# Kernel tuning notes

Measured on AMD Instinct MI355X. Metric: run time of the kernel, lower is better.

The kernel has to match this reference:

```python
import jax, jax.numpy as jnp
import numpy as np

# Hardcoded module dims (BClassifier: L=500, D=128, K=1; rehearsal_label=[0,1] => 2 classes)
L = 500
D = 128
NUM_CLASSES = 2
BUFFER_SIZE = 512
PER_CLS = BUFFER_SIZE // NUM_CLASSES  # 256
FEAT = 1024
B = 32
N = 4096
TEMP = 0.5
EPS = 1e-8  # torch cosine_similarity eps


def setup_inputs() -> dict:
    key = jax.random.key(0)
    ks = jax.random.split(key, 12)
    s = 0.02
    return {
        "x": jax.random.normal(ks[0], (B, N, FEAT), jnp.float32),
        "y": jax.random.randint(ks[1], (B,), 0, NUM_CLASSES),
        "W1": jax.random.normal(ks[2], (FEAT, L), jnp.float32) * s,
        "b1": jnp.zeros((L,), jnp.float32),
        "Wa": jax.random.normal(ks[3], (L, D), jnp.float32) * s,
        "ba": jnp.zeros((D,), jnp.float32),
        "Va": jax.random.normal(ks[4], (D, 1), jnp.float32) * s,
        "bv": jnp.zeros((1,), jnp.float32),
        "Wc": jax.random.normal(ks[5], (L, NUM_CLASSES), jnp.float32) * s,
        "bc": jnp.zeros((NUM_CLASSES,), jnp.float32),
        "rehearsal": jax.random.uniform(ks[6], (NUM_CLASSES, PER_CLS, L), jnp.float32),
    }


def _l2norm(v, axis=-1, keepdims=True):
    return jnp.maximum(jnp.linalg.norm(v, axis=axis, keepdims=keepdims), EPS)


def reference(x, y, W1, b1, Wa, ba, Va, bv, Wc, bc, rehearsal):
    # --- attention MIL pooling ---
    H = jax.nn.relu(jnp.einsum("bnf,fl->bnl", x, W1) + b1)          # [B,N,L]
    a = jax.nn.relu(jnp.einsum("bnl,ld->bnd", H, Wa) + ba) @ Va + bv  # [B,N,1]
    A = jax.nn.softmax(a[..., 0], axis=-1)                            # [B,N]
    bag_feat = jnp.einsum("bn,bnl->bl", A, H)                         # [B,L]
    logits_mlp = bag_feat @ Wc + bc                                   # [B,C]

    # --- buffer_update: contrastive loss + reg term ---
    cls_means = jnp.mean(rehearsal, axis=1)                           # [C,L]
    sim = bag_feat @ cls_means.T                                      # [B,C]
    pos = jnp.take_along_axis(sim, y[:, None], axis=1)                # [B,1]
    neg = jnp.take_along_axis(sim, (1 - y)[:, None], axis=1)          # [B,1] (C==2)
    logits = jnp.concatenate([pos, neg], axis=1)
    loss = -jnp.mean(jax.nn.log_softmax(logits / TEMP, axis=1)[:, 0])

    cm_n = cls_means / _l2norm(cls_means)                             # [C,L]
    cc = 1.0 + cm_n @ cm_n.T                                          # [C,C]
    reg = (jnp.sum(cc) - jnp.trace(cc)) / 2.0

    # --- sequential rehearsal scatter update ---
    reh_n = rehearsal / _l2norm(rehearsal)                            # [C,P,L]
    cls_dists = jnp.einsum("cl,cpl->cp", cm_n, reh_n)                 # [C,P]
    bag_n = bag_feat / _l2norm(bag_feat)                              # [B,L]

    def step(carry, inp):
        reh, dists = carry
        xi, xin, ci = inp
        d = jnp.dot(cm_n[ci], xin)                 # cos(cls_means[ci], x_i)
        row = dists[ci]
        idx = jnp.argmin(row)
        mv = row[idx]
        cond = d > mv
        reh = reh.at[ci, idx].set(jnp.where(cond, xi, reh[ci, idx]))
        dists = dists.at[ci, idx].set(jnp.where(cond, d, mv))
        return (reh, dists), None

    (new_rehearsal, _), _ = jax.lax.scan(step, (rehearsal, cls_dists), (bag_feat, bag_n, y))

    return logits_mlp, loss, reg, new_rehearsal
```

## Files before the change

kernel.cpp:

```cpp
#include <hip/hip_runtime.h>


#define EPSF 1e-8f

typedef float v4f __attribute__((ext_vector_type(4)));
typedef short v8s __attribute__((ext_vector_type(8)));

__device__ __forceinline__ unsigned short f2bf(float f) {
  unsigned u = __float_as_uint(f);
  u = (u + 0x7fffu + ((u >> 16) & 1u)) >> 16;
  return (unsigned short)u;
}
__device__ __forceinline__ float bf2f(unsigned short b) {
  return __uint_as_float(((unsigned)b) << 16);
}
__device__ __forceinline__ void gll16(const void* g, void* l) {
  __builtin_amdgcn_global_load_lds((const __attribute__((address_space(1))) void*)g,
                                   (__attribute__((address_space(3))) void*)l, 16, 0, 0);
}

__global__ void k0_w1t(const float* __restrict__ W1, unsigned short* __restrict__ W1T) {
  int idx = blockIdx.x * 256 + threadIdx.x;
  int n = idx >> 10, k = idx & 1023;
  float v = (n < 500) ? W1[k * 500 + n] : 0.f;
  W1T[idx] = f2bf(v);
}
__global__ void k0_wat(const float* __restrict__ Wa, unsigned short* __restrict__ WaT) {
  int idx = blockIdx.x * 256 + threadIdx.x;
  int d = idx >> 9, l = idx & 511;
  float v = (l < 500) ? Wa[l * 128 + d] : 0.f;
  WaT[idx] = f2bf(v);
}

__global__ __launch_bounds__(256) void k1_gemm1(const float* __restrict__ x,
    const unsigned short* __restrict__ W1T, const float* __restrict__ b1,
    unsigned short* __restrict__ H) {
  __shared__ float As[128 * 64];
  __shared__ unsigned short Bs[128 * 64];
  int bid = blockIdx.x;
  int n0 = (bid & 3) * 128;
  size_t m0 = (size_t)(bid >> 2) * 128;
  int tid = threadIdx.x;
  int lane = tid & 63, wv = tid >> 6;
  int wm = (wv >> 1) * 64, wn = (wv & 1) * 64;
  int l15 = lane & 15, quad = lane >> 4;
  v4f acc[4][4];
  for (int i = 0; i < 4; i++)
    for (int j = 0; j < 4; j++) acc[i][j] = (v4f)(0.f);

  for (int kt = 0; kt < 1024; kt += 64) {
    const float* gA = x + m0 * 1024 + kt;
    const unsigned short* gB = W1T + (size_t)n0 * 1024 + kt;
#pragma unroll
    for (int p = 0; p < 8; p++) {
      int ci = p * 256 + tid;
      gll16(gA + (size_t)(ci >> 4) * 1024 + (ci & 15) * 4, As + ci * 4);
    }
#pragma unroll
    for (int p = 0; p < 4; p++) {
      int ci = p * 256 + tid;
      gll16(gB + (size_t)(ci >> 3) * 1024 + (ci & 7) * 8, Bs + ci * 8);
    }
    __syncthreads();
#pragma unroll
    for (int kk = 0; kk < 64; kk += 32) {
      v8s af[4], bf[4];
#pragma unroll
      for (int mi = 0; mi < 4; mi++) {
        const float* p = As + (wm + mi * 16 + l15) * 64 + kk + quad * 8;
        v4f lo = *(const v4f*)p;
        v4f hi = *(const v4f*)(p + 4);
        v8s t;
        t[0] = (short)f2bf(lo.x); t[1] = (short)f2bf(lo.y);
        t[2] = (short)f2bf(lo.z); t[3] = (short)f2bf(lo.w);
        t[4] = (short)f2bf(hi.x); t[5] = (short)f2bf(hi.y);
        t[6] = (short)f2bf(hi.z); t[7] = (short)f2bf(hi.w);
        af[mi] = t;
      }
#pragma unroll
      for (int ni = 0; ni < 4; ni++)
        bf[ni] = *(const v8s*)(Bs + (wn + ni * 16 + l15) * 64 + kk + quad * 8);
#pragma unroll
      for (int mi = 0; mi < 4; mi++)
#pragma unroll
        for (int ni = 0; ni < 4; ni++)
          acc[mi][ni] = __builtin_amdgcn_mfma_f32_16x16x32_bf16(af[mi], bf[ni], acc[mi][ni], 0, 0, 0);
    }
    __syncthreads();
  }
#pragma unroll
  for (int mi = 0; mi < 4; mi++) {
#pragma unroll
    for (int ni = 0; ni < 4; ni++) {
      int col = n0 + wn + ni * 16 + l15;
      float bias = (col < 500) ? b1[col] : 0.f;
#pragma unroll
      for (int r = 0; r < 4; r++) {
        size_t row = m0 + wm + mi * 16 + quad * 4 + r;
        float v = (col < 500) ? fmaxf(acc[mi][ni][r] + bias, 0.f) : 0.f;
        H[row * 512 + col] = f2bf(v);
      }
    }
  }
}

__global__ __launch_bounds__(256) void k2_attn(const unsigned short* __restrict__ H,
    const unsigned short* __restrict__ WaT, const float* __restrict__ ba,
    const float* __restrict__ Va, const float* __restrict__ bv,
    float* __restrict__ aout) {
  __shared__ unsigned short Hs[128 * 64];
  __shared__ unsigned short Ws[128 * 64];
  size_t m0 = (size_t)blockIdx.x * 128;
  int tid = threadIdx.x;
  int lane = tid & 63, wv = tid >> 6;
  int wm = wv * 32;
  int l15 = lane & 15, quad = lane >> 4;
  v4f acc[2][8];
  for (int i = 0; i < 2; i++)
    for (int j = 0; j < 8; j++) acc[i][j] = (v4f)(0.f);

  for (int kt = 0; kt < 512; kt += 64) {
    const unsigned short* gH = H + m0 * 512 + kt;
    const unsigned short* gW = WaT + kt;
#pragma unroll
    for (int p = 0; p < 4; p++) {
      int ci = p * 256 + tid;
      gll16(gH + (size_t)(ci >> 3) * 512 + (ci & 7) * 8, Hs + ci * 8);
    }
#pragma unroll
    for (int p = 0; p < 4; p++) {
      int ci = p * 256 + tid;
      gll16(gW + (size_t)(ci >> 3) * 512 + (ci & 7) * 8, Ws + ci * 8);
    }
    __syncthreads();
#pragma unroll
    for (int kk = 0; kk < 64; kk += 32) {
      v8s af[2], bf[8];
#pragma unroll
      for (int mi = 0; mi < 2; mi++)
        af[mi] = *(const v8s*)(Hs + (wm + mi * 16 + l15) * 64 + kk + quad * 8);
#pragma unroll
      for (int ni = 0; ni < 8; ni++)
        bf[ni] = *(const v8s*)(Ws + (ni * 16 + l15) * 64 + kk + quad * 8);
#pragma unroll
      for (int mi = 0; mi < 2; mi++)
#pragma unroll
        for (int ni = 0; ni < 8; ni++)
          acc[mi][ni] = __builtin_amdgcn_mfma_f32_16x16x32_bf16(af[mi], bf[ni], acc[mi][ni], 0, 0, 0);
    }
    __syncthreads();
  }
  float bav[8], vav[8];
#pragma unroll
  for (int ni = 0; ni < 8; ni++) {
    int n = ni * 16 + l15;
    bav[ni] = ba[n];
    vav[ni] = Va[n];
  }
  float bv0 = bv[0];
#pragma unroll
  for (int mi = 0; mi < 2; mi++) {
#pragma unroll
    for (int r = 0; r < 4; r++) {
      float s = 0.f;
#pragma unroll
      for (int ni = 0; ni < 8; ni++) s += fmaxf(acc[mi][ni][r] + bav[ni], 0.f) * vav[ni];
      s += __shfl_xor(s, 1); s += __shfl_xor(s, 2);
      s += __shfl_xor(s, 4); s += __shfl_xor(s, 8);
      if (l15 == 0) aout[m0 + wm + mi * 16 + quad * 4 + r] = s + bv0;
    }
  }
}

__global__ void k3_softmax(float* __restrict__ a) {
  __shared__ float red[256];
  int b = blockIdx.x, tid = threadIdx.x;
  float* row = a + b * 4096;
  float m = -1e30f;
  for (int i = tid; i < 4096; i += 256) m = fmaxf(m, row[i]);
  red[tid] = m; __syncthreads();
  for (int s = 128; s > 0; s >>= 1) { if (tid < s) red[tid] = fmaxf(red[tid], red[tid + s]); __syncthreads(); }
  m = red[0]; __syncthreads();
  float sum = 0.f;
  for (int i = tid; i < 4096; i += 256) { float e = expf(row[i] - m); row[i] = e; sum += e; }
  red[tid] = sum; __syncthreads();
  for (int s = 128; s > 0; s >>= 1) { if (tid < s) red[tid] += red[tid + s]; __syncthreads(); }
  float inv = 1.f / red[0];
  for (int i = tid; i < 4096; i += 256) row[i] *= inv;
}

__global__ void k4_bag(const unsigned short* __restrict__ H, const float* __restrict__ A,
                       float* __restrict__ bag) {
  int bid = blockIdx.x;
  int b = bid >> 4, ch = bid & 15;
  int tid = threadIdx.x;
  size_t base = ((size_t)b * 4096 + ch * 256) * 512;
  const float* Ab = A + b * 4096 + ch * 256;
  float s0 = 0.f, s1 = 0.f;
  for (int n = 0; n < 256; n += 4) {
#pragma unroll
    for (int j = 0; j < 4; j++) {
      float w = Ab[n + j];
      unsigned hv = *(const unsigned*)(H + base + (size_t)(n + j) * 512 + tid * 2);
      s0 += w * bf2f((unsigned short)(hv & 0xffffu));
      s1 += w * bf2f((unsigned short)(hv >> 16));
    }
  }
  atomicAdd(&bag[b * 512 + tid * 2], s0);
  atomicAdd(&bag[b * 512 + tid * 2 + 1], s1);
}

__global__ void k5_copy(const float* __restrict__ reh, float* __restrict__ out) {
  int idx = blockIdx.x * 256 + threadIdx.x;
  if (idx < 256000) out[66 + idx] = reh[idx];
}

__global__ void k5_means(const float* __restrict__ reh, float* __restrict__ cm) {
  int idx = blockIdx.x * 256 + threadIdx.x;
  int c = idx >> 9, l = idx & 511;
  float s = 0.f;
  if (l < 500) {
    const float* p = reh + c * 128000 + l;
    for (int q = 0; q < 256; q++) s += p[q * 500];
    s *= (1.f / 256.f);
  }
  cm[idx] = s;
}

__global__ void k5_cmnorm(const float* __restrict__ cm, float* __restrict__ cmn) {
  __shared__ float red[256];
  int c = blockIdx.x, tid = threadIdx.x;
  float v = 0.f;
  for (int l = tid; l < 512; l += 256) { float x = cm[c * 512 + l]; v += x * x; }
  red[tid] = v; __syncthreads();
  for (int s = 128; s > 0; s >>= 1) { if (tid < s) red[tid] += red[tid + s]; __syncthreads(); }
  if (tid == 0) cmn[c] = sqrtf(red[0]);
}

__global__ void k5_dists(const float* __restrict__ reh, const float* __restrict__ cm,
                         const float* __restrict__ cmn, float* __restrict__ dists) {
  int bid = blockIdx.x;
  int c = bid >> 8, p = bid & 255;
  int lane = threadIdx.x;
  const float* row = reh + (c * 256 + p) * 500;
  const float* cmr = cm + c * 512;
  float dot = 0.f, n2 = 0.f;
  for (int l = lane; l < 500; l += 64) { float r = row[l]; dot += r * cmr[l]; n2 += r * r; }
#pragma unroll
  for (int m = 32; m > 0; m >>= 1) { dot += __shfl_xor(dot, m); n2 += __shfl_xor(n2, m); }
  if (lane == 0)
    dists[c * 256 + p] = dot / (fmaxf(cmn[c], EPSF) * fmaxf(sqrtf(n2), EPSF));
}

__global__ __launch_bounds__(256) void k5_head(const float* __restrict__ bag,
    const float* __restrict__ cm, const float* __restrict__ cmn,
    const float* __restrict__ distsIn, const int* __restrict__ y,
    const float* __restrict__ Wc, const float* __restrict__ bc,
    float* __restrict__ out) {
  __shared__ float simL[32][2], logitL[32][2], bagn[32];
  __shared__ float dists[512];
  __shared__ int owner[512];
  __shared__ float rv[256];
  __shared__ int ri[256];
  __shared__ float dot01S;
  int tid = threadIdx.x;
  int lane = tid & 63, wv = tid >> 6;
  for (int j = 0; j < 8; j++) {
    int b = wv * 8 + j;
    const float* br = bag + b * 512;
    float s0 = 0, s1 = 0, w0 = 0, w1 = 0, n2 = 0;
    for (int l = lane; l < 500; l += 64) {
      float v = br[l];
      s0 += v * cm[l]; s1 += v * cm[512 + l];
      w0 += v * Wc[l * 2]; w1 += v * Wc[l * 2 + 1];
      n2 += v * v;
    }
#pragma unroll
    for (int m = 32; m > 0; m >>= 1) {
      s0 += __shfl_xor(s0, m); s1 += __shfl_xor(s1, m);
      w0 += __shfl_xor(w0, m); w1 += __shfl_xor(w1, m);
      n2 += __shfl_xor(n2, m);
    }
    if (lane == 0) {
      simL[b][0] = s0; simL[b][1] = s1;
      logitL[b][0] = w0 + bc[0]; logitL[b][1] = w1 + bc[1];
      bagn[b] = sqrtf(n2);
    }
  }
  if (wv == 0) {
    float d = 0.f;
    for (int l = lane; l < 500; l += 64) d += cm[l] * cm[512 + l];
#pragma unroll
    for (int m = 32; m > 0; m >>= 1) d += __shfl_xor(d, m);
    if (lane == 0) dot01S = d;
  }
  dists[tid] = distsIn[tid]; dists[tid + 256] = distsIn[tid + 256];
  owner[tid] = -1; owner[tid + 256] = -1;
  __syncthreads();
  if (tid < 64) out[tid] = logitL[tid >> 1][tid & 1];
  if (tid == 0) {
    float acc = 0.f;
    for (int b = 0; b < 32; b++) {
      int yb = y[b];
      float p = simL[b][yb] * 2.0f;
      float ng = simL[b][1 - yb] * 2.0f;
      float mx = fmaxf(p, ng);
      float lse = mx + logf(expf(p - mx) + expf(ng - mx));
      acc += p - lse;
    }
    out[64] = -acc / 32.f;
    out[65] = 1.f + dot01S / (fmaxf(cmn[0], EPSF) * fmaxf(cmn[1], EPSF));
  }
  __syncthreads();
  for (int i = 0; i < 32; i++) {
    int ci = y[i];
    rv[tid] = dists[ci * 256 + tid]; ri[tid] = tid;
    __syncthreads();
    for (int s = 128; s > 0; s >>= 1) {
      if (tid < s) {
        float ov = rv[tid + s]; int oi = ri[tid + s];
        if (ov < rv[tid] || (ov == rv[tid] && oi < ri[tid])) { rv[tid] = ov; ri[tid] = oi; }
      }
      __syncthreads();
    }
    if (tid == 0) {
      float mv = rv[0]; int idx = ri[0];
      float d = simL[i][ci] / (fmaxf(cmn[ci], EPSF) * fmaxf(bagn[i], EPSF));
      if (d > mv) { dists[ci * 256 + idx] = d; owner[ci * 256 + idx] = i; }
    }
    __syncthreads();
  }
  for (int s = 0; s < 512; s++) {
    int o = owner[s];
    if (o >= 0)
      for (int l = tid; l < 500; l += 256) out[66 + s * 500 + l] = bag[o * 512 + l];
  }
}

extern "C" void kernel_launch(void* const* d_in, const int* in_sizes, int n_in,
                              void* d_out, int out_size, void* d_ws, size_t ws_size,
                              hipStream_t stream) {
  const float* x  = (const float*)d_in[0];
  const int*   y  = (const int*)d_in[1];
  const float* W1 = (const float*)d_in[2];
  const float* b1 = (const float*)d_in[3];
  const float* Wa = (const float*)d_in[4];
  const float* ba = (const float*)d_in[5];
  const float* Va = (const float*)d_in[6];
  const float* bv = (const float*)d_in[7];
  const float* Wc = (const float*)d_in[8];
  const float* bc = (const float*)d_in[9];
  const float* reh = (const float*)d_in[10];
  float* out = (float*)d_out;

  char* ws = (char*)d_ws;
  unsigned short* H   = (unsigned short*)ws;
  float*          a   = (float*)(ws + 134217728);
  unsigned short* W1T = (unsigned short*)(ws + 134742016);
  unsigned short* WaT = (unsigned short*)(ws + 135790592);
  float*          bag = (float*)(ws + 135921664);
  float*          cm  = (float*)(ws + 135987200);
  float*          cmn = (float*)(ws + 135991296);
  float*          dst = (float*)(ws + 135991552);

  hipMemsetAsync(bag, 0, 65536, stream);
  k0_w1t<<<2048, 256, 0, stream>>>(W1, W1T);
  k0_wat<<<256, 256, 0, stream>>>(Wa, WaT);
  k1_gemm1<<<4096, 256, 0, stream>>>(x, W1T, b1, H);
  k2_attn<<<1024, 256, 0, stream>>>(H, WaT, ba, Va, bv, a);
  k3_softmax<<<32, 256, 0, stream>>>(a);
  k4_bag<<<512, 256, 0, stream>>>(H, a, bag);
  k5_copy<<<1001, 256, 0, stream>>>(reh, out);
  k5_means<<<4, 256, 0, stream>>>(reh, cm);
  k5_cmnorm<<<2, 256, 0, stream>>>(cm, cmn);
  k5_dists<<<512, 64, 0, stream>>>(reh, cm, cmn, dst);
  k5_head<<<1, 256, 0, stream>>>(bag, cm, cmn, dst, y, Wc, bc, out);
}
```

Measured before the change: 1.163 ms.

## Swizzle LDS tiles, remap GEMM block order, and move rehearsal argmin to one wavefront

Applies an XOR swizzle to the LDS layouts in both MFMA GEMM kernels to remove bank conflicts, and uses perm-based bf16 packing (truncation instead of round-to-nearest) in the fp32-to-bf16 conversion. Reorders GEMM1 block indices so blocks running at the same time share W1 column tiles across M rows. Rewrites the class-means kernel to read rows coalesced, and replaces the barrier-heavy shared-memory argmin loop in the head kernel with a single-wavefront register and shuffle reduction. Truncating instead of rounding slightly changes numerics.

```diff
diff --git a/kernel.cpp b/kernel.cpp
--- a/kernel.cpp
+++ b/kernel.cpp
@@ -13,6 +13,9 @@
 }
 __device__ __forceinline__ float bf2f(unsigned short b) {
   return __uint_as_float(((unsigned)b) << 16);
+}
+__device__ __forceinline__ unsigned pk(float a, float b) {
+  return __builtin_amdgcn_perm(__float_as_uint(b), __float_as_uint(a), 0x07060302u);
 }
 __device__ __forceinline__ void gll16(const void* g, void* l) {
   __builtin_amdgcn_global_load_lds((const __attribute__((address_space(1))) void*)g,
@@ -38,15 +41,17 @@
   __shared__ float As[128 * 64];
   __shared__ unsigned short Bs[128 * 64];
   int bid = blockIdx.x;
-  int n0 = (bid & 3) * 128;
-  size_t m0 = (size_t)(bid >> 2) * 128;
+  int x8 = bid & 7, j = bid >> 3;
+  int mb = x8 * 128 + (j >> 2);
+  int n0 = (j & 3) * 128;
+  size_t m0 = (size_t)mb * 128;
   int tid = threadIdx.x;
   int lane = tid & 63, wv = tid >> 6;
   int wm = (wv >> 1) * 64, wn = (wv & 1) * 64;
-  int l15 = lane & 15, quad = lane >> 4;
+  int l15 = lane & 15, quad = lane >> 4, m7 = l15 & 7;
   v4f acc[4][4];
   for (int i = 0; i < 4; i++)
-    for (int j = 0; j < 4; j++) acc[i][j] = (v4f)(0.f);
+    for (int jj = 0; jj < 4; jj++) acc[i][jj] = (v4f)(0.f);
 
   for (int kt = 0; kt < 1024; kt += 64) {
     const float* gA = x + m0 * 1024 + kt;
@@ -54,32 +59,36 @@
 #pragma unroll
     for (int p = 0; p < 8; p++) {
       int ci = p * 256 + tid;
-      gll16(gA + (size_t)(ci >> 4) * 1024 + (ci & 15) * 4, As + ci * 4);
+      int r = ci >> 4, pc = ci & 15;
+      int c = pc ^ (r & 7);
+      gll16(gA + (size_t)r * 1024 + c * 4, As + ci * 4);
     }
 #pragma unroll
     for (int p = 0; p < 4; p++) {
       int ci = p * 256 + tid;
-      gll16(gB + (size_t)(ci >> 3) * 1024 + (ci & 7) * 8, Bs + ci * 8);
+      int r = ci >> 3, pc = ci & 7;
+      int c = pc ^ (r & 7);
+      gll16(gB + (size_t)r * 1024 + c * 8, Bs + ci * 8);
     }
     __syncthreads();
 #pragma unroll
     for (int kk = 0; kk < 64; kk += 32) {
       v8s af[4], bf[4];
+      int c0 = (kk >> 2) + 2 * quad;
+      int cb = (kk >> 3) + quad;
 #pragma unroll
       for (int mi = 0; mi < 4; mi++) {
-        const float* p = As + (wm + mi * 16 + l15) * 64 + kk + quad * 8;
-        v4f lo = *(const v4f*)p;
-        v4f hi = *(const v4f*)(p + 4);
-        v8s t;
-        t[0] = (short)f2bf(lo.x); t[1] = (short)f2bf(lo.y);
-        t[2] = (short)f2bf(lo.z); t[3] = (short)f2bf(lo.w);
-        t[4] = (short)f2bf(hi.x); t[5] = (short)f2bf(hi.y);
-        t[6] = (short)f2bf(hi.z); t[7] = (short)f2bf(hi.w);
-        af[mi] = t;
+        const float* rowp = As + (wm + mi * 16 + l15) * 64;
+        v4f lo = *(const v4f*)(rowp + ((c0 ^ m7) << 2));
+        v4f hi = *(const v4f*)(rowp + (((c0 + 1) ^ m7) << 2));
+        union { unsigned u[4]; v8s v; } t;
+        t.u[0] = pk(lo.x, lo.y); t.u[1] = pk(lo.z, lo.w);
+        t.u[2] = pk(hi.x, hi.y); t.u[3] = pk(hi.z, hi.w);
+        af[mi] = t.v;
       }
 #pragma unroll
       for (int ni = 0; ni < 4; ni++)
-        bf[ni] = *(const v8s*)(Bs + (wn + ni * 16 + l15) * 64 + kk + quad * 8);
+        bf[ni] = *(const v8s*)(Bs + (wn + ni * 16 + l15) * 64 + ((cb ^ m7) << 3));
 #pragma unroll
       for (int mi = 0; mi < 4; mi++)
 #pragma unroll
@@ -114,10 +123,10 @@
   int tid = threadIdx.x;
   int lane = tid & 63, wv = tid >> 6;
   int wm = wv * 32;
-  int l15 = lane & 15, quad = lane >> 4;
+  int l15 = lane & 15, quad = lane >> 4, m7 = l15 & 7;
   v4f acc[2][8];
   for (int i = 0; i < 2; i++)
-    for (int j = 0; j < 8; j++) acc[i][j] = (v4f)(0.f);
+    for (int jj = 0; jj < 8; jj++) acc[i][jj] = (v4f)(0.f);
 
   for (int kt = 0; kt < 512; kt += 64) {
     const unsigned short* gH = H + m0 * 512 + kt;
@@ -125,23 +134,28 @@
 #pragma unroll
     for (int p = 0; p < 4; p++) {
       int ci = p * 256 + tid;
-      gll16(gH + (size_t)(ci >> 3) * 512 + (ci & 7) * 8, Hs + ci * 8);
+      int r = ci >> 3, pc = ci & 7;
+      int c = pc ^ (r & 7);
+      gll16(gH + (size_t)r * 512 + c * 8, Hs + ci * 8);
     }
 #pragma unroll
     for (int p = 0; p < 4; p++) {
       int ci = p * 256 + tid;
-      gll16(gW + (size_t)(ci >> 3) * 512 + (ci & 7) * 8, Ws + ci * 8);
+      int r = ci >> 3, pc = ci & 7;
+      int c = pc ^ (r & 7);
+      gll16(gW + (size_t)r * 512 + c * 8, Ws + ci * 8);
     }
     __syncthreads();
 #pragma unroll
     for (int kk = 0; kk < 64; kk += 32) {
       v8s af[2], bf[8];
+      int cb = (kk >> 3) + quad;
 #pragma unroll
       for (int mi = 0; mi < 2; mi++)
-        af[mi] = *(const v8s*)(Hs + (wm + mi * 16 + l15) * 64 + kk + quad * 8);
+        af[mi] = *(const v8s*)(Hs + (wm + mi * 16 + l15) * 64 + ((cb ^ m7) << 3));
 #pragma unroll
       for (int ni = 0; ni < 8; ni++)
-        bf[ni] = *(const v8s*)(Ws + (ni * 16 + l15) * 64 + kk + quad * 8);
+        bf[ni] = *(const v8s*)(Ws + (ni * 16 + l15) * 64 + ((cb ^ m7) << 3));
 #pragma unroll
       for (int mi = 0; mi < 2; mi++)
 #pragma unroll
@@ -199,9 +213,9 @@
   float s0 = 0.f, s1 = 0.f;
   for (int n = 0; n < 256; n += 4) {
 #pragma unroll
-    for (int j = 0; j < 4; j++) {
-      float w = Ab[n + j];
-      unsigned hv = *(const unsigned*)(H + base + (size_t)(n + j) * 512 + tid * 2);
+    for (int jj = 0; jj < 4; jj++) {
+      float w = Ab[n + jj];
+      unsigned hv = *(const unsigned*)(H + base + (size_t)(n + jj) * 512 + tid * 2);
       s0 += w * bf2f((unsigned short)(hv & 0xffffu));
       s1 += w * bf2f((unsigned short)(hv >> 16));
     }
@@ -216,22 +230,24 @@
 }
 
 __global__ void k5_means(const float* __restrict__ reh, float* __restrict__ cm) {
-  int idx = blockIdx.x * 256 + threadIdx.x;
-  int c = idx >> 9, l = idx & 511;
-  float s = 0.f;
-  if (l < 500) {
-    const float* p = reh + c * 128000 + l;
-    for (int q = 0; q < 256; q++) s += p[q * 500];
-    s *= (1.f / 256.f);
-  }
-  cm[idx] = s;
+  int c = blockIdx.x, tid = threadIdx.x;
+  const float* base = reh + c * 128000;
+  float s0 = 0.f, s1 = 0.f;
+  for (int q = 0; q < 256; q++) {
+    const float* row = base + q * 500;
+    s0 += row[tid];
+    if (tid + 256 < 500) s1 += row[tid + 256];
+  }
+  cm[c * 512 + tid] = s0 * (1.f / 256.f);
+  int l2 = tid + 256;
+  cm[c * 512 + l2] = (l2 < 500) ? s1 * (1.f / 256.f) : 0.f;
 }
 
 __global__ void k5_cmnorm(const float* __restrict__ cm, float* __restrict__ cmn) {
   __shared__ float red[256];
   int c = blockIdx.x, tid = threadIdx.x;
   float v = 0.f;
-  for (int l = tid; l < 512; l += 256) { float x = cm[c * 512 + l]; v += x * x; }
+  for (int l = tid; l < 512; l += 256) { float xx = cm[c * 512 + l]; v += xx * xx; }
   red[tid] = v; __syncthreads();
   for (int s = 128; s > 0; s >>= 1) { if (tid < s) red[tid] += red[tid + s]; __syncthreads(); }
   if (tid == 0) cmn[c] = sqrtf(red[0]);
@@ -258,10 +274,7 @@
     const float* __restrict__ Wc, const float* __restrict__ bc,
     float* __restrict__ out) {
   __shared__ float simL[32][2], logitL[32][2], bagn[32];
-  __shared__ float dists[512];
-  __shared__ int owner[512];
-  __shared__ float rv[256];
-  __shared__ int ri[256];
+  __shared__ int ownS[512];
   __shared__ float dot01S;
   int tid = threadIdx.x;
   int lane = tid & 63, wv = tid >> 6;
@@ -287,18 +300,16 @@
       bagn[b] = sqrtf(n2);
     }
   }
-  if (wv == 0) {
+  if (wv == 1) {
     float d = 0.f;
     for (int l = lane; l < 500; l += 64) d += cm[l] * cm[512 + l];
 #pragma unroll
     for (int m = 32; m > 0; m >>= 1) d += __shfl_xor(d, m);
     if (lane == 0) dot01S = d;
   }
-  dists[tid] = distsIn[tid]; dists[tid + 256] = distsIn[tid + 256];
-  owner[tid] = -1; owner[tid + 256] = -1;
   __syncthreads();
   if (tid < 64) out[tid] = logitL[tid >> 1][tid & 1];
-  if (tid == 0) {
+  if (tid == 64) {
     float acc = 0.f;
     for (int b = 0; b < 32; b++) {
       int yb = y[b];
@@ -311,27 +322,36 @@
     out[64] = -acc / 32.f;
     out[65] = 1.f + dot01S / (fmaxf(cmn[0], EPSF) * fmaxf(cmn[1], EPSF));
   }
+  if (wv == 0) {
+    float dreg[8]; int oreg[8];
+#pragma unroll
+    for (int j = 0; j < 8; j++) { dreg[j] = distsIn[j * 64 + lane]; oreg[j] = -1; }
+    for (int i = 0; i < 32; i++) {
+      int ci = y[i];
+      int jb = ci * 4;
+      float v = dreg[jb]; int p = lane;
+#pragma unroll
+      for (int jj = 1; jj < 4; jj++) {
+        float nv = dreg[jb + jj]; int np = jj * 64 + lane;
+        if (nv < v || (nv == v && np < p)) { v = nv; p = np; }
+      }
+#pragma unroll
+      for (int s = 1; s < 64; s <<= 1) {
+        float ov = __shfl_xor(v, s); int op = __shfl_xor(p, s);
+        if (ov < v || (ov == v && op < p)) { v = ov; p = op; }
+      }
+      float d = simL[i][ci] / (fmaxf(cmn[ci], EPSF) * fmaxf(bagn[i], EPSF));
+      if (d > v && (p & 63) == lane) {
+        int jj = jb + (p >> 6);
+        dreg[jj] = d; oreg[jj] = i;
+      }
+    }
+#pragma unroll
+    for (int j = 0; j < 8; j++) ownS[j * 64 + lane] = oreg[j];
+  }
   __syncthreads();
-  for (int i = 0; i < 32; i++) {
-    int ci = y[i];
-    rv[tid] = dists[ci * 256 + tid]; ri[tid] = tid;
-    __syncthreads();
-    for (int s = 128; s > 0; s >>= 1) {
-      if (tid < s) {
-        float ov = rv[tid + s]; int oi = ri[tid + s];
-        if (ov < rv[tid] || (ov == rv[tid] && oi < ri[tid])) { rv[tid] = ov; ri[tid] = oi; }
-      }
-      __syncthreads();
-    }
-    if (tid == 0) {
-      float mv = rv[0]; int idx = ri[0];
-      float d = simL[i][ci] / (fmaxf(cmn[ci], EPSF) * fmaxf(bagn[i], EPSF));
-      if (d > mv) { dists[ci * 256 + idx] = d; owner[ci * 256 + idx] = i; }
-    }
-    __syncthreads();
-  }
   for (int s = 0; s < 512; s++) {
-    int o = owner[s];
+    int o = ownS[s];
     if (o >= 0)
       for (int l = tid; l < 500; l += 256) out[66 + s * 500 + l] = bag[o * 512 + l];
   }
@@ -371,7 +391,7 @@
   k3_softmax<<<32, 256, 0, stream>>>(a);
   k4_bag<<<512, 256, 0, stream>>>(H, a, bag);
   k5_copy<<<1001, 256, 0, stream>>>(reh, out);
-  k5_means<<<4, 256, 0, stream>>>(reh, cm);
+  k5_means<<<2, 256, 0, stream>>>(reh, cm);
   k5_cmnorm<<<2, 256, 0, stream>>>(cm, cmn);
   k5_dists<<<512, 64, 0, stream>>>(reh, cm, cmn, dst);
   k5_head<<<1, 256, 0, stream>>>(bag, cm, cmn, dst, y, Wc, bc, out);
```

Result: faster. 1.080 ms (-7.1%).
